# Kernel tuning notes

Hardware: AMD Instinct MI355X
Metric: run time of the kernel (lower is better)

## Reference

```python
import jax, jax.numpy as jnp
import numpy as np

N, C, H, W = 512, 2048, 16, 8
NUM_CLASSES = 751
ALPHA = 1.2      # margin
LAMB = 0.5       # self.l
SIGMA = 0.8      # osm_sigma
BN_EPS = 1e-5


def setup_inputs() -> dict:
    key = jax.random.key(0)
    k1, k2, k3 = jax.random.split(key, 3)
    features = jax.random.normal(k1, (N, C, H, W), dtype=jnp.float32)
    targets = jax.random.randint(k2, (N,), 0, NUM_CLASSES)
    gamma = jnp.ones((C,), dtype=jnp.float32)  # BN weight, init 1 (weights_init_kaiming)
    # kaiming_uniform_(a=sqrt(5)) on [NUM_CLASSES, C]: bound = 1/sqrt(C)
    bound = 1.0 / np.sqrt(C)
    weight = jax.random.uniform(k3, (NUM_CLASSES, C), jnp.float32, -bound, bound)
    return {"features": features, "targets": targets, "gamma": gamma, "weight": weight}


def _l2norm(x, axis=-1):
    return x / jnp.maximum(jnp.linalg.norm(x, axis=axis, keepdims=True), 1e-12)


def reference(features, targets, gamma, weight):
    n = features.shape[0]
    # AdaptiveAvgPool2d(1) + Flatten
    global_feat = jnp.mean(features, axis=(2, 3))  # [n, C]
    # NoBiasBatchNorm1d (training mode: batch stats, biased var, no bias)
    mu = jnp.mean(global_feat, axis=0)
    var = jnp.var(global_feat, axis=0)
    bn_feat = (global_feat - mu) / jnp.sqrt(var + BN_EPS) * gamma
    bn_feat = _l2norm(bn_feat, axis=1)  # F.normalize

    # pairwise euclidean distance
    sq = jnp.sum(bn_feat * bn_feat, axis=1)                       # [n]
    dist2 = sq[:, None] + sq[None, :] - 2.0 * (bn_feat @ bn_feat.T)
    dist = jnp.sqrt(jnp.clip(dist2, 1e-12, None))                 # [n, n]

    S_pos = jnp.exp(-(dist * dist) / (SIGMA * SIGMA))
    S_neg = jnp.clip(ALPHA - dist, 1e-12, None)
    p_mask = targets[:, None] == targets[None, :]                 # [n, n] bool
    S = jnp.where(p_mask, S_pos, S_neg)

    # per-sample attention: exp(logits)[i, t_i] / sum_j exp(logits)[i, j] == softmax
    logits = bn_feat @ _l2norm(weight, axis=1).T                  # [n, num_classes]
    probs = jax.nn.softmax(logits, axis=1)
    atten = probs[jnp.arange(n), targets]                         # [n]
    A = jnp.minimum(atten[None, :], atten[:, None])               # [n, n]

    Wmat = S * A
    off_diag = 1.0 - jnp.eye(n, dtype=Wmat.dtype)
    W_P = Wmat * p_mask.astype(Wmat.dtype) * off_diag
    W_N = Wmat * (~p_mask).astype(Wmat.dtype) * off_diag

    L_P = 0.5 * jnp.sum(W_P * dist * dist) / jnp.sum(W_P)
    L_N = 0.5 * jnp.sum(W_N * S_neg * S_neg) / jnp.sum(W_N)
    L = (1.0 - LAMB) * L_P + LAMB * L_N
    return (L, global_feat)
```

## Files before the change

kernel.cpp:

```cpp
#include <hip/hip_runtime.h>
#include <hip/hip_bf16.h>
#include <math.h>

#define N_S   512
#define C_S   2048
#define HW_S  128
#define NCLS  751
#define NCLSP 768
#define ALPHA 1.2f
#define LAMB  0.5f
#define SIGMA 0.8f
#define BN_EPS 1e-5f
#define KSPLIT 4
#define KSEG  (C_S / KSPLIT)

typedef __attribute__((ext_vector_type(8))) short short8;
typedef __attribute__((ext_vector_type(4))) float f32x4;

__device__ __forceinline__ unsigned short f2bf(float x) {
    __hip_bfloat16 h = __float2bfloat16(x);
    return *reinterpret_cast<unsigned short*>(&h);
}

__global__ __launch_bounds__(256) void pool_kernel(const float* __restrict__ feat,
                                                   float* __restrict__ out_gf,
                                                   float* __restrict__ ctrl) {
    if (blockIdx.x == 0 && threadIdx.x < 8) ctrl[threadIdx.x] = 0.0f;
    int pair = blockIdx.x * 32 + (threadIdx.x >> 3);
    int sub  = threadIdx.x & 7;
    const float4* p = reinterpret_cast<const float4*>(feat + (size_t)pair * HW_S);
    float4 v0 = p[sub];
    float4 v1 = p[sub + 8];
    float4 v2 = p[sub + 16];
    float4 v3 = p[sub + 24];
    float s = (v0.x + v0.y + v0.z + v0.w) + (v1.x + v1.y + v1.z + v1.w)
            + (v2.x + v2.y + v2.z + v2.w) + (v3.x + v3.y + v3.z + v3.w);
    #pragma unroll
    for (int off = 4; off > 0; off >>= 1) s += __shfl_down(s, off, 8);
    if (sub == 0) out_gf[pair] = s * (1.0f / HW_S);
}

__global__ __launch_bounds__(256) void meanvar_kernel(const float* __restrict__ gf,
                                                      const float* __restrict__ gamma,
                                                      float* __restrict__ mu_out,
                                                      float* __restrict__ scale_out) {
    int tc = threadIdx.x & 31;
    int tr = threadIdx.x >> 5;
    int c  = blockIdx.x * 32 + tc;
    const float* col = gf + c;
    float sum = 0.f, sumsq = 0.f;
    #pragma unroll 4
    for (int n = tr * 64; n < tr * 64 + 64; ++n) {
        float x = col[(size_t)n * C_S];
        sum += x; sumsq += x * x;
    }
    __shared__ float s1[8][32], s2[8][32];
    s1[tr][tc] = sum; s2[tr][tc] = sumsq;
    __syncthreads();
    if (threadIdx.x < 32) {
        int cc = blockIdx.x * 32 + threadIdx.x;
        float a = 0.f, b = 0.f;
        #pragma unroll
        for (int r = 0; r < 8; ++r) { a += s1[r][threadIdx.x]; b += s2[r][threadIdx.x]; }
        float mu  = a * (1.0f / N_S);
        float var = b * (1.0f / N_S) - mu * mu;
        mu_out[cc]    = mu;
        scale_out[cc] = gamma[cc] / sqrtf(var + BN_EPS);
    }
}

__global__ __launch_bounds__(256) void norm_kernel(const float* __restrict__ gf,
                                                   const float* __restrict__ mu,
                                                   const float* __restrict__ scale,
                                                   const float* __restrict__ w,
                                                   unsigned short* __restrict__ bnnh,
                                                   unsigned short* __restrict__ wnh,
                                                   float* __restrict__ sq) {
    int b = blockIdx.x, t = threadIdx.x;
    __shared__ float red[4];
    __shared__ float sinv;
    if (b < N_S) {
        int n = b;
        const float* row = gf + (size_t)n * C_S;
        float v[8]; float ss = 0.f;
        #pragma unroll
        for (int k = 0; k < 8; ++k) {
            int c = t + k * 256;
            float x = (row[c] - mu[c]) * scale[c];
            v[k] = x; ss += x * x;
        }
        #pragma unroll
        for (int off = 32; off > 0; off >>= 1) ss += __shfl_down(ss, off, 64);
        if ((t & 63) == 0) red[t >> 6] = ss;
        __syncthreads();
        if (t == 0) {
            float tot = red[0] + red[1] + red[2] + red[3];
            float inv = 1.0f / fmaxf(sqrtf(tot), 1e-12f);
            sinv = inv;
            sq[n] = tot * inv * inv;
        }
        __syncthreads();
        float inv = sinv;
        unsigned short* orow = bnnh + (size_t)n * C_S;
        #pragma unroll
        for (int k = 0; k < 8; ++k) orow[t + k * 256] = f2bf(v[k] * inv);
    } else {
        int r = b - N_S;
        unsigned short* orow = wnh + (size_t)r * C_S;
        if (r >= NCLS) {
            #pragma unroll
            for (int k = 0; k < 8; ++k) orow[t + k * 256] = 0;
            return;
        }
        const float* row = w + (size_t)r * C_S;
        float v[8]; float ss = 0.f;
        #pragma unroll
        for (int k = 0; k < 8; ++k) {
            float x = row[t + k * 256];
            v[k] = x; ss += x * x;
        }
        #pragma unroll
        for (int off = 32; off > 0; off >>= 1) ss += __shfl_down(ss, off, 64);
        if ((t & 63) == 0) red[t >> 6] = ss;
        __syncthreads();
        if (t == 0) sinv = 1.0f / fmaxf(sqrtf(red[0]+red[1]+red[2]+red[3]), 1e-12f);
        __syncthreads();
        float inv = sinv;
        #pragma unroll
        for (int k = 0; k < 8; ++k) orow[t + k * 256] = f2bf(v[k] * inv);
    }
}

__global__ __launch_bounds__(256) void gemm_kernel(const unsigned short* __restrict__ bnnh,
                                                   const unsigned short* __restrict__ wnh,
                                                   float* __restrict__ logits_p,
                                                   float* __restrict__ G_p) {
    int wave = threadIdx.x >> 6, lane = threadIdx.x & 63;
    int gid = blockIdx.x * 4 + wave;
    const unsigned short* Bh; float* Cm; int m0, n0, ldc, ks;
    if (gid < 1536) {
        int tile = gid >> 2; ks = gid & 3;
        Bh = wnh; m0 = (tile & 31) * 16; n0 = (tile >> 5) * 64; ldc = NCLSP;
        Cm = logits_p + (size_t)ks * (N_S * NCLSP);
    } else {
        int g2 = gid - 1536;
        int tile = g2 >> 2; ks = g2 & 3;
        Bh = bnnh; m0 = (tile & 31) * 16; n0 = (tile >> 5) * 64; ldc = N_S;
        Cm = G_p + (size_t)ks * (N_S * N_S);
    }
    int kbase = ks * KSEG;
    int mrow = m0 + (lane & 15);
    int kq   = (lane >> 4) * 8;
    f32x4 acc0 = {0,0,0,0}, acc1 = {0,0,0,0}, acc2 = {0,0,0,0}, acc3 = {0,0,0,0};
    const unsigned short* arow = bnnh + (size_t)mrow * C_S + kbase + kq;
    const unsigned short* brow = Bh + (size_t)(n0 + (lane & 15)) * C_S + kbase + kq;
    #pragma unroll 2
    for (int k = 0; k < KSEG; k += 32) {
        short8 a  = *reinterpret_cast<const short8*>(arow + k);
        short8 b0 = *reinterpret_cast<const short8*>(brow + k);
        short8 b1 = *reinterpret_cast<const short8*>(brow + 16 * C_S + k);
        short8 b2 = *reinterpret_cast<const short8*>(brow + 32 * C_S + k);
        short8 b3 = *reinterpret_cast<const short8*>(brow + 48 * C_S + k);
        acc0 = __builtin_amdgcn_mfma_f32_16x16x32_bf16(a, b0, acc0, 0, 0, 0);
        acc1 = __builtin_amdgcn_mfma_f32_16x16x32_bf16(a, b1, acc1, 0, 0, 0);
        acc2 = __builtin_amdgcn_mfma_f32_16x16x32_bf16(a, b2, acc2, 0, 0, 0);
        acc3 = __builtin_amdgcn_mfma_f32_16x16x32_bf16(a, b3, acc3, 0, 0, 0);
    }
    int ccol  = lane & 15;
    int crow0 = m0 + (lane >> 4) * 4;
    #pragma unroll
    for (int r = 0; r < 4; ++r) {
        float* orow = Cm + (size_t)(crow0 + r) * ldc + n0 + ccol;
        orow[0]  = acc0[r];
        orow[16] = acc1[r];
        orow[32] = acc2[r];
        orow[48] = acc3[r];
    }
}

__global__ __launch_bounds__(256) void softmax_atten_kernel(const float* __restrict__ logits_p,
                                                            const int* __restrict__ targets,
                                                            float* __restrict__ atten) {
    int n = blockIdx.x, t = threadIdx.x;
    const float* r0 = logits_p + (size_t)n * NCLSP;
    const float* r1 = r0 + (size_t)(N_S * NCLSP);
    const float* r2 = r1 + (size_t)(N_S * NCLSP);
    const float* r3 = r2 + (size_t)(N_S * NCLSP);
    __shared__ float red[4];
    __shared__ float srmax, srsum;
    float m = -1e30f;
    for (int k = t; k < NCLS; k += 256) m = fmaxf(m, r0[k] + r1[k] + r2[k] + r3[k]);
    #pragma unroll
    for (int off = 32; off > 0; off >>= 1) m = fmaxf(m, __shfl_down(m, off, 64));
    if ((t & 63) == 0) red[t >> 6] = m;
    __syncthreads();
    if (t == 0) srmax = fmaxf(fmaxf(red[0], red[1]), fmaxf(red[2], red[3]));
    __syncthreads();
    float rm = srmax;
    float s = 0.f;
    for (int k = t; k < NCLS; k += 256) s += expf(r0[k] + r1[k] + r2[k] + r3[k] - rm);
    #pragma unroll
    for (int off = 32; off > 0; off >>= 1) s += __shfl_down(s, off, 64);
    if ((t & 63) == 0) red[t >> 6] = s;
    __syncthreads();
    if (t == 0) {
        srsum = red[0] + red[1] + red[2] + red[3];
        int tg = targets[n];
        atten[n] = expf(r0[tg] + r1[tg] + r2[tg] + r3[tg] - rm) / srsum;
    }
}

__global__ __launch_bounds__(256) void pair_reduce_kernel(const float* __restrict__ G_p,
                                                          const float* __restrict__ sq,
                                                          const float* __restrict__ atten,
                                                          const int* __restrict__ targets,
                                                          float* __restrict__ ctrl,
                                                          float* __restrict__ out) {
    float numP = 0.f, denP = 0.f, numN = 0.f, denN = 0.f;
    const float inv_sig2 = 1.0f / (SIGMA * SIGMA);
    const float* G0 = G_p;
    const float* G1 = G0 + N_S * N_S;
    const float* G2 = G1 + N_S * N_S;
    const float* G3 = G2 + N_S * N_S;
    for (int p = blockIdx.x * 256 + threadIdx.x; p < N_S * N_S; p += 256 * 256) {
        int i = p >> 9, j = p & (N_S - 1);
        if (i == j) continue;
        float g    = G0[p] + G1[p] + G2[p] + G3[p];
        float d2   = fmaxf(sq[i] + sq[j] - 2.0f * g, 1e-12f);
        float dist = sqrtf(d2);
        float sneg = fmaxf(ALPHA - dist, 1e-12f);
        float Aij  = fminf(atten[i], atten[j]);
        if (targets[i] == targets[j]) {
            float Wm = expf(-d2 * inv_sig2) * Aij;
            numP += Wm * d2; denP += Wm;
        } else {
            float Wm = sneg * Aij;
            numN += Wm * sneg * sneg; denN += Wm;
        }
    }
    #pragma unroll
    for (int off = 32; off > 0; off >>= 1) {
        numP += __shfl_down(numP, off, 64);
        denP += __shfl_down(denP, off, 64);
        numN += __shfl_down(numN, off, 64);
        denN += __shfl_down(denN, off, 64);
    }
    __shared__ float red[4][4];
    int t = threadIdx.x;
    if ((t & 63) == 0) {
        int w = t >> 6;
        red[w][0] = numP; red[w][1] = denP; red[w][2] = numN; red[w][3] = denN;
    }
    __syncthreads();
    if (t < 4) {
        float s = red[0][t] + red[1][t] + red[2][t] + red[3][t];
        atomicAdd(&ctrl[t], s);
    }
    __syncthreads();
    if (t == 0) {
        __threadfence();
        unsigned prev = atomicAdd(reinterpret_cast<unsigned*>(ctrl + 4), 1u);
        if (prev == gridDim.x - 1) {
            float a0 = atomicAdd(&ctrl[0], 0.0f);
            float a1 = atomicAdd(&ctrl[1], 0.0f);
            float a2 = atomicAdd(&ctrl[2], 0.0f);
            float a3 = atomicAdd(&ctrl[3], 0.0f);
            float L_P = 0.5f * a0 / a1;
            float L_N = 0.5f * a2 / a3;
            out[0] = (1.0f - LAMB) * L_P + LAMB * L_N;
        }
    }
}

extern "C" void kernel_launch(void* const* d_in, const int* in_sizes, int n_in,
                              void* d_out, int out_size, void* d_ws, size_t ws_size,
                              hipStream_t stream) {
    const float* features = (const float*)d_in[0];
    const int*   targets  = (const int*)d_in[1];
    const float* gamma    = (const float*)d_in[2];
    const float* weight   = (const float*)d_in[3];
    float* out = (float*)d_out;
    float* gf  = out + 1;

    float* ws       = (float*)d_ws;
    float* mu       = ws;
    float* scale    = mu + 2048;
    float* sq       = scale + 2048;
    float* atten    = sq + 512;
    float* ctrl     = atten + 512;
    float* logits_p = ctrl + 16;
    float* G_p      = logits_p + 4 * (N_S * NCLSP);
    unsigned short* bnnh = (unsigned short*)(G_p + 4 * (N_S * N_S));
    unsigned short* wnh  = bnnh + (size_t)N_S * C_S;

    hipLaunchKernelGGL(pool_kernel, dim3((N_S * C_S) / 32), dim3(256), 0, stream,
                       features, gf, ctrl);
    hipLaunchKernelGGL(meanvar_kernel, dim3(C_S / 32), dim3(256), 0, stream,
                       gf, gamma, mu, scale);
    hipLaunchKernelGGL(norm_kernel, dim3(N_S + NCLSP), dim3(256), 0, stream,
                       gf, mu, scale, weight, bnnh, wnh, sq);
    hipLaunchKernelGGL(gemm_kernel, dim3(640), dim3(256), 0, stream,
                       bnnh, wnh, logits_p, G_p);
    hipLaunchKernelGGL(softmax_atten_kernel, dim3(N_S), dim3(256), 0, stream,
                       logits_p, targets, atten);
    hipLaunchKernelGGL(pair_reduce_kernel, dim3(256), dim3(256), 0, stream,
                       G_p, sq, atten, targets, ctrl, out);
}
```

Baseline: 735.4 us.

## Vectorize softmax and pair reduction, use nontemporal pool loads, unroll GEMM further

The pooling kernel now reads features with nontemporal vector loads so the large one-pass stream does not pollute the cache. The softmax kernel loads each row as one float4 per thread, keeps the values in registers and captures the target element during the exp pass, so the partial logits are not reread. The pair reduction kernel maps each thread to four consecutive columns with vector loads of G, sq, atten and targets, replacing the strided scalar loop. The MFMA GEMM loop unroll goes from 2 to 4, which may raise register pressure.

Measured after the change: 708.1 us. -3.7%, faster.

```diff
diff --git a/kernel.cpp b/kernel.cpp
--- a/kernel.cpp
+++ b/kernel.cpp
@@ -28,13 +28,13 @@
     if (blockIdx.x == 0 && threadIdx.x < 8) ctrl[threadIdx.x] = 0.0f;
     int pair = blockIdx.x * 32 + (threadIdx.x >> 3);
     int sub  = threadIdx.x & 7;
-    const float4* p = reinterpret_cast<const float4*>(feat + (size_t)pair * HW_S);
-    float4 v0 = p[sub];
-    float4 v1 = p[sub + 8];
-    float4 v2 = p[sub + 16];
-    float4 v3 = p[sub + 24];
-    float s = (v0.x + v0.y + v0.z + v0.w) + (v1.x + v1.y + v1.z + v1.w)
-            + (v2.x + v2.y + v2.z + v2.w) + (v3.x + v3.y + v3.z + v3.w);
+    const f32x4* p = reinterpret_cast<const f32x4*>(feat + (size_t)pair * HW_S);
+    f32x4 v0 = __builtin_nontemporal_load(p + sub);
+    f32x4 v1 = __builtin_nontemporal_load(p + sub + 8);
+    f32x4 v2 = __builtin_nontemporal_load(p + sub + 16);
+    f32x4 v3 = __builtin_nontemporal_load(p + sub + 24);
+    float s = (v0[0] + v0[1] + v0[2] + v0[3]) + (v1[0] + v1[1] + v1[2] + v1[3])
+            + (v2[0] + v2[1] + v2[2] + v2[3]) + (v3[0] + v3[1] + v3[2] + v3[3]);
     #pragma unroll
     for (int off = 4; off > 0; off >>= 1) s += __shfl_down(s, off, 8);
     if (sub == 0) out_gf[pair] = s * (1.0f / HW_S);
@@ -154,7 +154,7 @@
     f32x4 acc0 = {0,0,0,0}, acc1 = {0,0,0,0}, acc2 = {0,0,0,0}, acc3 = {0,0,0,0};
     const unsigned short* arow = bnnh + (size_t)mrow * C_S + kbase + kq;
     const unsigned short* brow = Bh + (size_t)(n0 + (lane & 15)) * C_S + kbase + kq;
-    #pragma unroll 2
+    #pragma unroll 4
     for (int k = 0; k < KSEG; k += 32) {
         short8 a  = *reinterpret_cast<const short8*>(arow + k);
         short8 b0 = *reinterpret_cast<const short8*>(brow + k);
@@ -182,14 +182,25 @@
                                                             const int* __restrict__ targets,
                                                             float* __restrict__ atten) {
     int n = blockIdx.x, t = threadIdx.x;
-    const float* r0 = logits_p + (size_t)n * NCLSP;
-    const float* r1 = r0 + (size_t)(N_S * NCLSP);
-    const float* r2 = r1 + (size_t)(N_S * NCLSP);
-    const float* r3 = r2 + (size_t)(N_S * NCLSP);
+    const f32x4* r0 = reinterpret_cast<const f32x4*>(logits_p + (size_t)n * NCLSP);
+    const f32x4* r1 = r0 + (size_t)(N_S * NCLSP) / 4;
+    const f32x4* r2 = r1 + (size_t)(N_S * NCLSP) / 4;
+    const f32x4* r3 = r2 + (size_t)(N_S * NCLSP) / 4;
     __shared__ float red[4];
-    __shared__ float srmax, srsum;
+    __shared__ float srmax, srsum, stgt;
+    const bool has = (t < NCLSP / 4);
+    f32x4 v = {-1e30f, -1e30f, -1e30f, -1e30f};
     float m = -1e30f;
-    for (int k = t; k < NCLS; k += 256) m = fmaxf(m, r0[k] + r1[k] + r2[k] + r3[k]);
+    if (has) {
+        f32x4 a = r0[t], b = r1[t], c = r2[t], d = r3[t];
+        v = a + b + c + d;
+        int base = t * 4;
+        if (base + 0 >= NCLS) v[0] = -1e30f;
+        if (base + 1 >= NCLS) v[1] = -1e30f;
+        if (base + 2 >= NCLS) v[2] = -1e30f;
+        if (base + 3 >= NCLS) v[3] = -1e30f;
+        m = fmaxf(fmaxf(v[0], v[1]), fmaxf(v[2], v[3]));
+    }
     #pragma unroll
     for (int off = 32; off > 0; off >>= 1) m = fmaxf(m, __shfl_down(m, off, 64));
     if ((t & 63) == 0) red[t >> 6] = m;
@@ -197,16 +208,26 @@
     if (t == 0) srmax = fmaxf(fmaxf(red[0], red[1]), fmaxf(red[2], red[3]));
     __syncthreads();
     float rm = srmax;
+    int tg = targets[n];
     float s = 0.f;
-    for (int k = t; k < NCLS; k += 256) s += expf(r0[k] + r1[k] + r2[k] + r3[k] - rm);
+    if (has) {
+        float ex = expf(v[0] - rm);
+        float ey = expf(v[1] - rm);
+        float ez = expf(v[2] - rm);
+        float ew = expf(v[3] - rm);
+        s = ex + ey + ez + ew;
+        if (t == (tg >> 2)) {
+            int e = tg & 3;
+            stgt = (e == 0) ? ex : (e == 1) ? ey : (e == 2) ? ez : ew;
+        }
+    }
     #pragma unroll
     for (int off = 32; off > 0; off >>= 1) s += __shfl_down(s, off, 64);
     if ((t & 63) == 0) red[t >> 6] = s;
     __syncthreads();
     if (t == 0) {
         srsum = red[0] + red[1] + red[2] + red[3];
-        int tg = targets[n];
-        atten[n] = expf(r0[tg] + r1[tg] + r2[tg] + r3[tg] - rm) / srsum;
+        atten[n] = stgt / srsum;
     }
 }
 
@@ -218,19 +239,33 @@
                                                           float* __restrict__ out) {
     float numP = 0.f, denP = 0.f, numN = 0.f, denN = 0.f;
     const float inv_sig2 = 1.0f / (SIGMA * SIGMA);
-    const float* G0 = G_p;
-    const float* G1 = G0 + N_S * N_S;
-    const float* G2 = G1 + N_S * N_S;
-    const float* G3 = G2 + N_S * N_S;
-    for (int p = blockIdx.x * 256 + threadIdx.x; p < N_S * N_S; p += 256 * 256) {
-        int i = p >> 9, j = p & (N_S - 1);
-        if (i == j) continue;
-        float g    = G0[p] + G1[p] + G2[p] + G3[p];
-        float d2   = fmaxf(sq[i] + sq[j] - 2.0f * g, 1e-12f);
+    int g  = blockIdx.x * 256 + threadIdx.x;
+    int i  = g >> 7;
+    int j0 = (g & 127) * 4;
+    size_t p = (size_t)i * N_S + j0;
+    const f32x4* G0 = reinterpret_cast<const f32x4*>(G_p + p);
+    const f32x4* G1 = reinterpret_cast<const f32x4*>(G_p + N_S * N_S + p);
+    const f32x4* G2 = reinterpret_cast<const f32x4*>(G_p + 2 * N_S * N_S + p);
+    const f32x4* G3 = reinterpret_cast<const f32x4*>(G_p + 3 * N_S * N_S + p);
+    f32x4 gsumv = *G0 + *G1 + *G2 + *G3;
+    float gsum[4] = { gsumv[0], gsumv[1], gsumv[2], gsumv[3] };
+    f32x4 sqjv = *reinterpret_cast<const f32x4*>(sq + j0);
+    float sqj[4] = { sqjv[0], sqjv[1], sqjv[2], sqjv[3] };
+    f32x4 ajv = *reinterpret_cast<const f32x4*>(atten + j0);
+    float aj[4] = { ajv[0], ajv[1], ajv[2], ajv[3] };
+    int4 tjv = *reinterpret_cast<const int4*>(targets + j0);
+    int tj[4] = { tjv.x, tjv.y, tjv.z, tjv.w };
+    float sqi = sq[i];
+    float ai  = atten[i];
+    int   ti  = targets[i];
+    #pragma unroll
+    for (int e = 0; e < 4; ++e) {
+        if (i == j0 + e) continue;
+        float d2   = fmaxf(sqi + sqj[e] - 2.0f * gsum[e], 1e-12f);
         float dist = sqrtf(d2);
         float sneg = fmaxf(ALPHA - dist, 1e-12f);
-        float Aij  = fminf(atten[i], atten[j]);
-        if (targets[i] == targets[j]) {
+        float Aij  = fminf(ai, aj[e]);
+        if (ti == tj[e]) {
             float Wm = expf(-d2 * inv_sig2) * Aij;
             numP += Wm * d2; denP += Wm;
         } else {
```
